# Kernel optimization log

Hardware: AMD Instinct MI355X
Metric: run time of the kernel (lower is better)

## Reference

```python
import jax, jax.numpy as jnp
import numpy as np

EPS = 1e-5
P, B, T, C = 2, 8, 1024, 1024
H = 4 * C

def layernorm(x, g, b):
    mu = jnp.mean(x, axis=-1, keepdims=True)
    var = jnp.var(x, axis=-1, keepdims=True)
    return (x - mu) * jax.lax.rsqrt(var + EPS) * g + b

def time_shift(x):
    # ZeroPad2d((0,0,1,-1)): xx[t] = x[t-1], xx[0] = 0 along the T axis
    pad = [(0, 0)] * (x.ndim - 2) + [(1, 0), (0, 0)]
    return jnp.pad(x, pad)[..., :-1, :]

def wkv(time_decay, time_first, k, v):
    # Faithful port of the RWKV-v4 CUDA WKV scan (numerically stable form).
    # k, v: [N, T, C]; time_decay/time_first: [C]
    w = -jnp.exp(time_decay)  # decay (negative)
    u = time_first
    kT = jnp.moveaxis(k, 1, 0)  # [T, N, C]
    vT = jnp.moveaxis(v, 1, 0)
    N = k.shape[0]
    Cc = k.shape[2]

    def step(carry, kv):
        aa, bb, pp = carry
        kk, vv = kv
        ww = u + kk
        p = jnp.maximum(pp, ww)
        e1 = jnp.exp(pp - p)
        e2 = jnp.exp(ww - p)
        y = (e1 * aa + e2 * vv) / (e1 * bb + e2)
        ww2 = w + pp
        p2 = jnp.maximum(ww2, kk)
        e1b = jnp.exp(ww2 - p2)
        e2b = jnp.exp(kk - p2)
        return (e1b * aa + e2b * vv, e1b * bb + e2b, p2), y

    init = (jnp.zeros((N, Cc), jnp.float32), jnp.zeros((N, Cc), jnp.float32),
            jnp.full((N, Cc), -1e38, jnp.float32))
    _, yT = jax.lax.scan(step, init, (kT, vT))
    return jnp.moveaxis(yT, 0, 1)  # [N, T, C]


def setup_inputs() -> dict:
    key = jax.random.key(0)
    ks = jax.random.split(key, 20)
    f32 = jnp.float32
    layer_id, n_layer = 1, 12
    ratio_0_to_1 = layer_id / (n_layer - 1)
    ratio_1_to_almost0 = 1.0 - layer_id / n_layer
    xcurve = (np.arange(C, dtype=np.float32) / C).reshape(1, 1, C)
    decay_speed = -5 + 8 * (np.arange(C, dtype=np.float32) / (C - 1)) ** (0.7 + 1.3 * ratio_0_to_1)
    zigzag = (np.array([(i + 1) % 3 - 1 for i in range(C)], dtype=np.float32)) * 0.5
    time_first = np.ones(C, dtype=np.float32) * np.log(0.3) + zigzag
    mk = np.stack([xcurve ** ratio_1_to_almost0 for _ in range(P)], 0)  # [P,1,1,C]
    mv = np.stack([xcurve ** ratio_1_to_almost0 + 0.3 * ratio_0_to_1 for _ in range(P)], 0)
    mr = np.stack([xcurve ** (0.5 * ratio_1_to_almost0) for _ in range(P)], 0)
    s = 0.02
    return {
        'x': jax.random.normal(ks[0], (P, B, T, C), f32),
        'ln1_g': jnp.ones((C,), f32), 'ln1_b': jnp.zeros((C,), f32),
        'ln2_g': jnp.ones((C,), f32), 'ln2_b': jnp.zeros((C,), f32),
        'time_decay': jnp.asarray(decay_speed, f32),
        'time_first': jnp.asarray(time_first, f32),
        'att_mix_k': jnp.asarray(mk, f32), 'att_mix_v': jnp.asarray(mv, f32),
        'att_mix_r': jnp.asarray(mr, f32),
        'Wk': jax.random.normal(ks[1], (C, C), f32) * s,
        'Wv': jax.random.normal(ks[2], (C, C), f32) * s,
        'Wr': jax.random.normal(ks[3], (C, C), f32) * s,
        'Wo': jax.random.normal(ks[4], (C, C), f32) * s,
        'cm_mix_k': jnp.asarray(mk, f32), 'cm_mix_r': jnp.asarray(mk, f32),
        'Wck': jax.random.normal(ks[5], (H, C), f32) * s,
        'Wcr': jax.random.normal(ks[6], (C, C), f32) * s,
        'Wcv': jax.random.normal(ks[7], (C, H), f32) * s,
    }


def reference(x, ln1_g, ln1_b, ln2_g, ln2_b, time_decay, time_first,
              att_mix_k, att_mix_v, att_mix_r, Wk, Wv, Wr, Wo,
              cm_mix_k, cm_mix_r, Wck, Wcr, Wcv):
    p, b, t, c = x.shape
    # --- TimeMix branch: x = x + Wo @ (sigmoid(r) * WKV(k, v)) ---
    h = layernorm(x, ln1_g, ln1_b)
    xx = time_shift(h)
    xk = h * att_mix_k + xx * (1 - att_mix_k)
    xv = h * att_mix_v + xx * (1 - att_mix_v)
    xr = h * att_mix_r + xx * (1 - att_mix_r)
    k = jnp.einsum('pbtc,dc->pbtd', xk, Wk)
    v = jnp.einsum('pbtc,dc->pbtd', xv, Wv)
    sr = jax.nn.sigmoid(jnp.einsum('pbtc,dc->pbtd', xr, Wr))
    y = wkv(time_decay, time_first,
            k.reshape(p * b, t, c), v.reshape(p * b, t, c)).reshape(p, b, t, c)
    x = x + jnp.einsum('pbtc,dc->pbtd', sr * y, Wo)
    # --- ChannelMix branch ---
    h = layernorm(x, ln2_g, ln2_b)
    xx = time_shift(h)
    xk = h * cm_mix_k + xx * (1 - cm_mix_k)
    xr = h * cm_mix_r + xx * (1 - cm_mix_r)
    kk = jnp.einsum('pbtc,hc->pbth', xk, Wck)
    kk = jnp.square(jax.nn.relu(kk))
    kv = jnp.einsum('pbth,ch->pbtc', kk, Wcv)
    out = jax.nn.sigmoid(jnp.einsum('pbtc,dc->pbtd', xr, Wcr)) * kv
    return x + out
```

## Files before the change

### kernel.cpp

```cpp
#include <hip/hip_runtime.h>

#define T_SEQ 1024
#define C_DIM 1024
#define H_DIM 4096
#define M_ROWS 16384
#define CHUNKS 16
#define CLEN 64

typedef _Float16 f16x8 __attribute__((ext_vector_type(8)));
typedef _Float16 f16x4 __attribute__((ext_vector_type(4)));
typedef float    f32x4 __attribute__((ext_vector_type(4)));

#define AS1 __attribute__((address_space(1)))
#define AS3 __attribute__((address_space(3)))

__device__ __forceinline__ void gload_lds16(const void* g, void* l) {
  __builtin_amdgcn_global_load_lds((const AS1 void*)g, (AS3 void*)l, 16, 0, 0);
}

__device__ __forceinline__ float sigmoidf_(float x) {
  return 1.0f / (1.0f + __expf(-x));
}

struct CvtArgs {
  const float* src[7];
  _Float16*    dst[7];
  int n4[7];
  int start[8];
};

__global__ __launch_bounds__(256) void cvt_all_kernel(CvtArgs a) {
  const int bid = blockIdx.x;
  int s = 0;
#pragma unroll
  for (int j = 0; j < 7; ++j) s += (bid >= a.start[j + 1]) ? 1 : 0;
  const int i = (bid - a.start[s]) * 256 + threadIdx.x;
  if (i >= a.n4[s]) return;
  f32x4 v = reinterpret_cast<const f32x4*>(a.src[s])[i];
  f16x4 o;
  o[0] = (_Float16)v[0]; o[1] = (_Float16)v[1];
  o[2] = (_Float16)v[2]; o[3] = (_Float16)v[3];
  reinterpret_cast<f16x4*>(a.dst[s])[i] = o;
}

__global__ __launch_bounds__(256) void ln_kernel(const float* __restrict__ x,
    const float* __restrict__ g, const float* __restrict__ b,
    _Float16* __restrict__ h) {
  const int row  = blockIdx.x * 4 + (threadIdx.x >> 6);
  const int lane = threadIdx.x & 63;
  const f32x4* xr = reinterpret_cast<const f32x4*>(x + (size_t)row * C_DIM);
  f32x4 v[4];
  float s = 0.f, sq = 0.f;
#pragma unroll
  for (int i = 0; i < 4; ++i) {
    v[i] = xr[i * 64 + lane];
#pragma unroll
    for (int j = 0; j < 4; ++j) { s += v[i][j]; sq += v[i][j] * v[i][j]; }
  }
#pragma unroll
  for (int off = 32; off > 0; off >>= 1) {
    s  += __shfl_xor(s, off, 64);
    sq += __shfl_xor(sq, off, 64);
  }
  const float mu   = s * (1.0f / C_DIM);
  const float var  = sq * (1.0f / C_DIM) - mu * mu;
  const float rstd = rsqrtf(var + 1e-5f);
  const f32x4* g4 = reinterpret_cast<const f32x4*>(g);
  const f32x4* b4 = reinterpret_cast<const f32x4*>(b);
  f16x4* h4 = reinterpret_cast<f16x4*>(h + (size_t)row * C_DIM);
#pragma unroll
  for (int i = 0; i < 4; ++i) {
    f32x4 gg = g4[i * 64 + lane];
    f32x4 bb = b4[i * 64 + lane];
    f16x4 o;
#pragma unroll
    for (int j = 0; j < 4; ++j)
      o[j] = (_Float16)((v[i][j] - mu) * rstd * gg[j] + bb[j]);
    h4[i * 64 + lane] = o;
  }
}

__global__ __launch_bounds__(256) void mix3_kernel(const _Float16* __restrict__ h,
    const float* __restrict__ mk, const float* __restrict__ mv, const float* __restrict__ mr,
    _Float16* __restrict__ xk, _Float16* __restrict__ xv, _Float16* __restrict__ xr) {
  const int i  = blockIdx.x * 256 + threadIdx.x;
  const int m  = i >> 7;
  const int c0 = (i & 127) << 3;
  const int p  = m >> 13;
  const int t  = m & (T_SEQ - 1);
  const f16x8* h8 = reinterpret_cast<const f16x8*>(h);
  f16x8 hc = h8[i];
  f16x8 hp;
#pragma unroll
  for (int j = 0; j < 8; ++j) hp[j] = (_Float16)0.f;
  if (t) hp = h8[i - 128];
  f16x8 ok, ov, orr;
#pragma unroll
  for (int j = 0; j < 8; ++j) {
    const float hcf = (float)hc[j], hpf = (float)hp[j];
    const float a = mk[p * C_DIM + c0 + j];
    const float c = mv[p * C_DIM + c0 + j];
    const float d = mr[p * C_DIM + c0 + j];
    ok[j]  = (_Float16)(hcf * a + hpf * (1.f - a));
    ov[j]  = (_Float16)(hcf * c + hpf * (1.f - c));
    orr[j] = (_Float16)(hcf * d + hpf * (1.f - d));
  }
  reinterpret_cast<f16x8*>(xk)[i] = ok;
  reinterpret_cast<f16x8*>(xv)[i] = ov;
  reinterpret_cast<f16x8*>(xr)[i] = orr;
}

__global__ __launch_bounds__(256) void mix2_kernel(const _Float16* __restrict__ h,
    const float* __restrict__ mk, const float* __restrict__ mr,
    _Float16* __restrict__ xk, _Float16* __restrict__ xr) {
  const int i  = blockIdx.x * 256 + threadIdx.x;
  const int m  = i >> 7;
  const int c0 = (i & 127) << 3;
  const int p  = m >> 13;
  const int t  = m & (T_SEQ - 1);
  const f16x8* h8 = reinterpret_cast<const f16x8*>(h);
  f16x8 hc = h8[i];
  f16x8 hp;
#pragma unroll
  for (int j = 0; j < 8; ++j) hp[j] = (_Float16)0.f;
  if (t) hp = h8[i - 128];
  f16x8 ok, orr;
#pragma unroll
  for (int j = 0; j < 8; ++j) {
    const float hcf = (float)hc[j], hpf = (float)hp[j];
    const float a = mk[p * C_DIM + c0 + j];
    const float d = mr[p * C_DIM + c0 + j];
    ok[j]  = (_Float16)(hcf * a + hpf * (1.f - a));
    orr[j] = (_Float16)(hcf * d + hpf * (1.f - d));
  }
  reinterpret_cast<f16x8*>(xk)[i] = ok;
  reinterpret_cast<f16x8*>(xr)[i] = orr;
}

__global__ __launch_bounds__(1024, 1) void wkv_kernel(const _Float16* __restrict__ k,
    const _Float16* __restrict__ v, const _Float16* __restrict__ r,
    const float* __restrict__ td, const float* __restrict__ tf,
    _Float16* __restrict__ a_out) {
  __shared__ float sA[CHUNKS][64];
  __shared__ float sB[CHUNKS][64];
  __shared__ float sP[CHUNKS][64];
  const int tid   = threadIdx.x;
  const int chunk = tid >> 6;
  const int ch    = tid & 63;
  const int n     = blockIdx.x >> 4;
  const int cg    = blockIdx.x & 15;
  const int c     = cg * 64 + ch;
  const float w = -__expf(td[c]);
  const float u = tf[c];
  const size_t cbase = (size_t)n * T_SEQ * C_DIM + (size_t)chunk * CLEN * C_DIM + c;

  float aa = 0.f, bb = 0.f, pp = -1e38f;
  for (int s = 0; s < CLEN; ++s) {
    const size_t idx = cbase + (size_t)s * C_DIM;
    const float kk = (float)k[idx];
    const float vv = (float)v[idx];
    const float ww2 = w + pp;
    const float p2  = fmaxf(ww2, kk);
    const float e1b = __expf(ww2 - p2);
    const float e2b = __expf(kk - p2);
    aa = e1b * aa + e2b * vv;
    bb = e1b * bb + e2b;
    pp = p2;
  }
  sA[chunk][ch] = aa; sB[chunk][ch] = bb; sP[chunk][ch] = pp;
  __syncthreads();

  if (chunk == 0) {
    float pa = 0.f, pb = 0.f, ppr = -1e38f;
    const float wL = w * (float)CLEN;
    for (int j = 0; j < CHUNKS; ++j) {
      const float la = sA[j][ch], lb = sB[j][ch], lp = sP[j][ch];
      sA[j][ch] = pa; sB[j][ch] = pb; sP[j][ch] = ppr;
      const float dp = wL + ppr;
      const float np = fmaxf(dp, lp);
      const float e1 = __expf(dp - np);
      const float e2 = __expf(lp - np);
      pa  = e1 * pa + e2 * la;
      pb  = e1 * pb + e2 * lb;
      ppr = np;
    }
  }
  __syncthreads();

  aa = sA[chunk][ch]; bb = sB[chunk][ch]; pp = sP[chunk][ch];
  for (int s = 0; s < CLEN; ++s) {
    const size_t idx = cbase + (size_t)s * C_DIM;
    const float kk = (float)k[idx];
    const float vv = (float)v[idx];
    const float ww = u + kk;
    const float p  = fmaxf(pp, ww);
    const float e1 = __expf(pp - p);
    const float e2 = __expf(ww - p);
    const float yv = __fdividef(e1 * aa + e2 * vv, e1 * bb + e2);
    const float sr = sigmoidf_((float)r[idx]);
    a_out[idx] = (_Float16)(sr * yv);
    const float ww2 = w + pp;
    const float p2  = fmaxf(ww2, kk);
    const float e1b = __expf(ww2 - p2);
    const float e2b = __expf(kk - p2);
    aa = e1b * aa + e2b * vv;
    bb = e1b * bb + e2b;
    pp = p2;
  }
}

#define GBAR() do { __builtin_amdgcn_sched_barrier(0); \
                    __builtin_amdgcn_s_barrier(); \
                    __builtin_amdgcn_sched_barrier(0); } while (0)
#define WVN(n) do { asm volatile("s_waitcnt vmcnt(" #n ")" ::: "memory"); \
                    __builtin_amdgcn_sched_barrier(0); } while (0)
#define WLN(n) do { asm volatile("s_waitcnt lgkmcnt(" #n ")" ::: "memory"); \
                    __builtin_amdgcn_sched_barrier(0); } while (0)
#define SCHED() __builtin_amdgcn_sched_barrier(0)
#define STAGE(op, SRC, row0, k0, bb) do { \
    _Pragma("unroll") \
    for (int c_ = 0; c_ < 2; ++c_) { \
      gload_lds16((SRC) + (size_t)((row0) + c_ * 64) * K + (k0), \
                  &lds[bb][op][((size_t)((row0) + c_ * 64) << 6) + dbase]); \
    } } while (0)
#define RD_AH(dst, mh) do { \
    _Pragma("unroll") for (int i_ = 0; i_ < 4; ++i_) \
    _Pragma("unroll") for (int k_ = 0; k_ < 2; ++k_) \
      dst[i_][k_] = *reinterpret_cast<const f16x8*>( \
        &lds[b][0][((wr * 128 + (mh) * 64 + i_ * 16 + frow) << 6) + \
                   (((k_ << 5) + fk) ^ fxorh)]); \
  } while (0)
#define RD_BALL() do { \
    _Pragma("unroll") for (int j_ = 0; j_ < 4; ++j_) \
    _Pragma("unroll") for (int k_ = 0; k_ < 2; ++k_) \
      bf[j_][k_] = *reinterpret_cast<const f16x8*>( \
        &lds[b][1][((wcn * 64 + j_ * 16 + frow) << 6) + \
                   (((k_ << 5) + fk) ^ fxorh)]); \
  } while (0)
#define MM32(src, mh) do { \
    __builtin_amdgcn_s_setprio(1); \
    _Pragma("unroll") for (int k_ = 0; k_ < 2; ++k_) \
    _Pragma("unroll") for (int i_ = 0; i_ < 4; ++i_) \
    _Pragma("unroll") for (int j_ = 0; j_ < 4; ++j_) \
      acc[(mh) * 4 + i_][j_] = __builtin_amdgcn_mfma_f32_16x16x32_f16( \
        src[i_][k_], bf[j_][k_], acc[(mh) * 4 + i_][j_], 0, 0, 0); \
    __builtin_amdgcn_s_setprio(0); \
  } while (0)

template<int EPI>
__global__ __launch_bounds__(512, 2) void gemm_nt_256(
    const _Float16* __restrict__ A, const _Float16* __restrict__ B,
    void* __restrict__ Cv, const float* __restrict__ X,
    const _Float16* __restrict__ KV, int M, int N, int K) {
  __shared__ _Float16 lds[2][2][256 * 64];
  const int tid  = threadIdx.x;
  const int wave = tid >> 6;
  const int lane = tid & 63;
  const int wr   = wave >> 2;
  const int wcn  = wave & 3;

  const unsigned nwx  = gridDim.x;
  const unsigned pery = gridDim.y >> 3;
  const unsigned id   = blockIdx.y * nwx + blockIdx.x;
  const unsigned xcd  = id & 7;
  const unsigned loc  = id >> 3;
  const size_t m0 = (size_t)(xcd * pery + loc / nwx) * 256;
  const size_t n0 = (size_t)(loc % nwx) * 256;

  const int srow  = tid >> 3;
  const int scolh = ((tid & 7) ^ (srow & 7)) << 3;
  const size_t dbase = (size_t)(srow & ~7) << 6;
  const _Float16* sA = A + (m0 + srow) * (size_t)K + scolh;
  const _Float16* sB = B + (n0 + srow) * (size_t)K + scolh;

  const int frow  = lane & 15;
  const int fk    = (lane >> 4) << 3;
  const int fxorh = (frow & 7) << 3;

  f32x4 acc[8][4];
#pragma unroll
  for (int i = 0; i < 8; ++i)
#pragma unroll
    for (int j = 0; j < 4; ++j) acc[i][j] = (f32x4){0.f, 0.f, 0.f, 0.f};

  STAGE(0, sA, 0, 0, 0); STAGE(0, sA, 128, 0, 0);
  STAGE(1, sB, 0, 0, 0); STAGE(1, sB, 128, 0, 0);

  const int NT = K >> 6;
  for (int t = 0; t < NT; ++t) {
    const int b  = t & 1;
    const int nb = b ^ 1;
    const int k1 = (t + 1) << 6;
    if (t + 1 < NT) {
      STAGE(0, sA, 0, k1, nb); STAGE(0, sA, 128, k1, nb);
      STAGE(1, sB, 0, k1, nb); STAGE(1, sB, 128, k1, nb);
      WVN(8);
    } else {
      WVN(0);
    }
    GBAR();
    f16x8 a0[4][2], a1[4][2], bf[4][2];
    RD_AH(a0, 0); RD_BALL();
    SCHED();
    RD_AH(a1, 1);
    WLN(8);
    MM32(a0, 0);
    WLN(0);
    MM32(a1, 1);
    GBAR();
  }

  const int ecol  = lane & 15;
  const int erow4 = (lane >> 4) * 4;
#pragma unroll
  for (int mf = 0; mf < 8; ++mf)
#pragma unroll
    for (int nf = 0; nf < 4; ++nf) {
      const size_t rbase = m0 + (size_t)(wr * 128 + mf * 16 + erow4);
      const size_t cc    = n0 + (size_t)(wcn * 64 + nf * 16 + ecol);
#pragma unroll
      for (int r = 0; r < 4; ++r) {
        const float val = acc[mf][nf][r];
        const size_t off = (rbase + r) * (size_t)N + cc;
        if constexpr (EPI == 0) {
          ((_Float16*)Cv)[off] = (_Float16)val;
        } else if constexpr (EPI == 1) {
          const float tq = fmaxf(val, 0.f);
          ((_Float16*)Cv)[off] = (_Float16)(tq * tq);
        } else if constexpr (EPI == 2) {
          ((float*)Cv)[off] = val + X[off];
        } else {
          ((float*)Cv)[off] = X[off] + sigmoidf_(val) * (float)KV[off];
        }
      }
    }
}

extern "C" void kernel_launch(void* const* d_in, const int* in_sizes, int n_in,
                              void* d_out, int out_size, void* d_ws, size_t ws_size,
                              hipStream_t stream) {
  const float* x      = (const float*)d_in[0];
  const float* ln1_g  = (const float*)d_in[1];
  const float* ln1_b  = (const float*)d_in[2];
  const float* ln2_g  = (const float*)d_in[3];
  const float* ln2_b  = (const float*)d_in[4];
  const float* tdec   = (const float*)d_in[5];
  const float* tfirst = (const float*)d_in[6];
  const float* amk    = (const float*)d_in[7];
  const float* amv    = (const float*)d_in[8];
  const float* amr    = (const float*)d_in[9];
  const float* Wk     = (const float*)d_in[10];
  const float* Wv     = (const float*)d_in[11];
  const float* Wr     = (const float*)d_in[12];
  const float* Wo     = (const float*)d_in[13];
  const float* cmk    = (const float*)d_in[14];
  const float* cmr    = (const float*)d_in[15];
  const float* Wck    = (const float*)d_in[16];
  const float* Wcr    = (const float*)d_in[17];
  const float* Wcv    = (const float*)d_in[18];

  char* ws = (char*)d_ws;
  const size_t SZ = (size_t)M_ROWS * C_DIM * sizeof(_Float16);
  _Float16* B0 = (_Float16*)(ws + 0 * SZ);
  _Float16* B1 = (_Float16*)(ws + 1 * SZ);
  _Float16* B2 = (_Float16*)(ws + 2 * SZ);
  _Float16* B3 = (_Float16*)(ws + 3 * SZ);
  _Float16* B4 = (_Float16*)(ws + 4 * SZ);
  _Float16* B5 = (_Float16*)(ws + 5 * SZ);
  _Float16* B6 = (_Float16*)(ws + 6 * SZ);
  _Float16* wWk  = (_Float16*)(ws + 7 * SZ);
  _Float16* wWv  = wWk  + (size_t)C_DIM * C_DIM;
  _Float16* wWr  = wWv  + (size_t)C_DIM * C_DIM;
  _Float16* wWo  = wWr  + (size_t)C_DIM * C_DIM;
  _Float16* wWcr = wWo  + (size_t)C_DIM * C_DIM;
  _Float16* wWck = wWcr + (size_t)C_DIM * C_DIM;
  _Float16* wWcv = wWck + (size_t)H_DIM * C_DIM;

  {
    CvtArgs a;
    const float* srcs[7] = {Wk, Wv, Wr, Wo, Wcr, Wck, Wcv};
    _Float16*    dsts[7] = {wWk, wWv, wWr, wWo, wWcr, wWck, wWcv};
    const size_t ns[7]   = {(size_t)C_DIM * C_DIM, (size_t)C_DIM * C_DIM,
                            (size_t)C_DIM * C_DIM, (size_t)C_DIM * C_DIM,
                            (size_t)C_DIM * C_DIM, (size_t)H_DIM * C_DIM,
                            (size_t)C_DIM * H_DIM};
    int st = 0;
    for (int j = 0; j < 7; ++j) {
      a.src[j] = srcs[j]; a.dst[j] = dsts[j];
      a.n4[j] = (int)(ns[j] / 4);
      a.start[j] = st;
      st += (a.n4[j] + 255) / 256;
    }
    a.start[7] = st;
    cvt_all_kernel<<<dim3(st), dim3(256), 0, stream>>>(a);
  }

  const dim3 blk(256);
  const dim3 gblk(512);
  const dim3 gN1(C_DIM / 256, M_ROWS / 256);
  const dim3 gN4(H_DIM / 256, M_ROWS / 256);

  ln_kernel<<<dim3(M_ROWS / 4), blk, 0, stream>>>(x, ln1_g, ln1_b, B0);
  mix3_kernel<<<dim3(M_ROWS * 128 / 256), blk, 0, stream>>>(B0, amk, amv, amr, B1, B2, B3);
  gemm_nt_256<0><<<gN1, gblk, 0, stream>>>(B1, wWk, B4, nullptr, nullptr, M_ROWS, C_DIM, C_DIM);
  gemm_nt_256<0><<<gN1, gblk, 0, stream>>>(B2, wWv, B5, nullptr, nullptr, M_ROWS, C_DIM, C_DIM);
  gemm_nt_256<0><<<gN1, gblk, 0, stream>>>(B3, wWr, B6, nullptr, nullptr, M_ROWS, C_DIM, C_DIM);
  wkv_kernel<<<dim3(256), dim3(1024), 0, stream>>>(B4, B5, B6, tdec, tfirst, B1);
  gemm_nt_256<2><<<gN1, gblk, 0, stream>>>(B1, wWo, d_out, x, nullptr, M_ROWS, C_DIM, C_DIM);

  ln_kernel<<<dim3(M_ROWS / 4), blk, 0, stream>>>((const float*)d_out, ln2_g, ln2_b, B0);
  mix2_kernel<<<dim3(M_ROWS * 128 / 256), blk, 0, stream>>>(B0, cmk, cmr, B1, B2);
  gemm_nt_256<1><<<gN4, gblk, 0, stream>>>(B1, wWck, B3, nullptr, nullptr, M_ROWS, H_DIM, C_DIM);
  gemm_nt_256<0><<<gN1, gblk, 0, stream>>>(B3, wWcv, B1, nullptr, nullptr, M_ROWS, C_DIM, H_DIM);
  gemm_nt_256<3><<<gN1, gblk, 0, stream>>>(B2, wWcr, d_out, (const float*)d_out, B1,
                                           M_ROWS, C_DIM, C_DIM);
}
```

Before: 668.6 us.

## Split GEMM main loop into four quadrant phases interleaving LDS staging with MFMA

Measured after the change: 659.0 us. No clear change (-1.4%).

```diff
diff --git a/kernel.cpp b/kernel.cpp
--- a/kernel.cpp
+++ b/kernel.cpp
@@ -216,7 +216,6 @@
                     __builtin_amdgcn_sched_barrier(0); } while (0)
 #define WLN(n) do { asm volatile("s_waitcnt lgkmcnt(" #n ")" ::: "memory"); \
                     __builtin_amdgcn_sched_barrier(0); } while (0)
-#define SCHED() __builtin_amdgcn_sched_barrier(0)
 #define STAGE(op, SRC, row0, k0, bb) do { \
     _Pragma("unroll") \
     for (int c_ = 0; c_ < 2; ++c_) { \
@@ -227,23 +226,23 @@
     _Pragma("unroll") for (int i_ = 0; i_ < 4; ++i_) \
     _Pragma("unroll") for (int k_ = 0; k_ < 2; ++k_) \
       dst[i_][k_] = *reinterpret_cast<const f16x8*>( \
-        &lds[b][0][((wr * 128 + (mh) * 64 + i_ * 16 + frow) << 6) + \
-                   (((k_ << 5) + fk) ^ fxorh)]); \
+        &lds[bi][0][((wr * 128 + (mh) * 64 + i_ * 16 + frow) << 6) + \
+                    (((k_ << 5) + fk) ^ fxorh)]); \
   } while (0)
-#define RD_BALL() do { \
-    _Pragma("unroll") for (int j_ = 0; j_ < 4; ++j_) \
+#define RD_BH(dst, nh) do { \
+    _Pragma("unroll") for (int j_ = 0; j_ < 2; ++j_) \
     _Pragma("unroll") for (int k_ = 0; k_ < 2; ++k_) \
-      bf[j_][k_] = *reinterpret_cast<const f16x8*>( \
-        &lds[b][1][((wcn * 64 + j_ * 16 + frow) << 6) + \
-                   (((k_ << 5) + fk) ^ fxorh)]); \
+      dst[j_][k_] = *reinterpret_cast<const f16x8*>( \
+        &lds[bi][1][((wcn * 64 + (nh) * 32 + j_ * 16 + frow) << 6) + \
+                    (((k_ << 5) + fk) ^ fxorh)]); \
   } while (0)
-#define MM32(src, mh) do { \
+#define MM16(asrc, bsrc, mh, nh) do { \
     __builtin_amdgcn_s_setprio(1); \
     _Pragma("unroll") for (int k_ = 0; k_ < 2; ++k_) \
     _Pragma("unroll") for (int i_ = 0; i_ < 4; ++i_) \
-    _Pragma("unroll") for (int j_ = 0; j_ < 4; ++j_) \
-      acc[(mh) * 4 + i_][j_] = __builtin_amdgcn_mfma_f32_16x16x32_f16( \
-        src[i_][k_], bf[j_][k_], acc[(mh) * 4 + i_][j_], 0, 0, 0); \
+    _Pragma("unroll") for (int j_ = 0; j_ < 2; ++j_) \
+      acc[(mh) * 4 + i_][(nh) * 2 + j_] = __builtin_amdgcn_mfma_f32_16x16x32_f16( \
+        asrc[i_][k_], bsrc[j_][k_], acc[(mh) * 4 + i_][(nh) * 2 + j_], 0, 0, 0); \
     __builtin_amdgcn_s_setprio(0); \
   } while (0)
 
@@ -288,25 +287,34 @@
 
   const int NT = K >> 6;
   for (int t = 0; t < NT; ++t) {
-    const int b  = t & 1;
-    const int nb = b ^ 1;
+    const int bi = t & 1;
+    const int nb = bi ^ 1;
     const int k1 = (t + 1) << 6;
-    if (t + 1 < NT) {
-      STAGE(0, sA, 0, k1, nb); STAGE(0, sA, 128, k1, nb);
-      STAGE(1, sB, 0, k1, nb); STAGE(1, sB, 128, k1, nb);
-      WVN(8);
-    } else {
-      WVN(0);
-    }
-    GBAR();
-    f16x8 a0[4][2], a1[4][2], bf[4][2];
-    RD_AH(a0, 0); RD_BALL();
-    SCHED();
-    RD_AH(a1, 1);
-    WLN(8);
-    MM32(a0, 0);
+    const bool st = (t + 1) < NT;
+    f16x8 af[4][2], b0f[2][2], b1f[2][2];
+    if (st) { STAGE(0, sA, 0, k1, nb); WVN(2); }
+    else    { WVN(0); }
+    GBAR();
+    RD_AH(af, 0); RD_BH(b0f, 0);
     WLN(0);
-    MM32(a1, 1);
+    MM16(af, b0f, 0, 0);
+    GBAR();
+    RD_BH(b1f, 1);
+    if (st) STAGE(1, sB, 0, k1, nb);
+    GBAR();
+    WLN(0);
+    MM16(af, b1f, 0, 1);
+    GBAR();
+    RD_AH(af, 1);
+    if (st) STAGE(1, sB, 128, k1, nb);
+    GBAR();
+    WLN(0);
+    MM16(af, b0f, 1, 0);
+    GBAR();
+    if (st) STAGE(0, sA, 128, k1, nb);
+    GBAR();
+    WLN(0);
+    MM16(af, b1f, 1, 1);
     GBAR();
   }
 
```

## Batch K/V/R projection GEMMs into one launch and interleave LDS reads with MFMAs

Applied to the files above, without the earlier changes.

Result: no change. 659.5 us (-1.4%).

```diff
diff --git a/kernel.cpp b/kernel.cpp
--- a/kernel.cpp
+++ b/kernel.cpp
@@ -223,27 +223,24 @@
       gload_lds16((SRC) + (size_t)((row0) + c_ * 64) * K + (k0), \
                   &lds[bb][op][((size_t)((row0) + c_ * 64) << 6) + dbase]); \
     } } while (0)
-#define RD_AH(dst, mh) do { \
+#define RD_A4(dst, mh, kk_) do { \
     _Pragma("unroll") for (int i_ = 0; i_ < 4; ++i_) \
-    _Pragma("unroll") for (int k_ = 0; k_ < 2; ++k_) \
-      dst[i_][k_] = *reinterpret_cast<const f16x8*>( \
-        &lds[b][0][((wr * 128 + (mh) * 64 + i_ * 16 + frow) << 6) + \
-                   (((k_ << 5) + fk) ^ fxorh)]); \
+      dst[i_][kk_] = *reinterpret_cast<const f16x8*>( \
+        &lds[bi][0][((wr * 128 + (mh) * 64 + i_ * 16 + frow) << 6) + \
+                    ((((kk_) << 5) + fk) ^ fxorh)]); \
   } while (0)
-#define RD_BALL() do { \
+#define RD_B4(kk_) do { \
     _Pragma("unroll") for (int j_ = 0; j_ < 4; ++j_) \
-    _Pragma("unroll") for (int k_ = 0; k_ < 2; ++k_) \
-      bf[j_][k_] = *reinterpret_cast<const f16x8*>( \
-        &lds[b][1][((wcn * 64 + j_ * 16 + frow) << 6) + \
-                   (((k_ << 5) + fk) ^ fxorh)]); \
+      bf[j_][kk_] = *reinterpret_cast<const f16x8*>( \
+        &lds[bi][1][((wcn * 64 + j_ * 16 + frow) << 6) + \
+                    ((((kk_) << 5) + fk) ^ fxorh)]); \
   } while (0)
-#define MM32(src, mh) do { \
+#define MMC(asrc, kk_, half) do { \
     __builtin_amdgcn_s_setprio(1); \
-    _Pragma("unroll") for (int k_ = 0; k_ < 2; ++k_) \
     _Pragma("unroll") for (int i_ = 0; i_ < 4; ++i_) \
     _Pragma("unroll") for (int j_ = 0; j_ < 4; ++j_) \
-      acc[(mh) * 4 + i_][j_] = __builtin_amdgcn_mfma_f32_16x16x32_f16( \
-        src[i_][k_], bf[j_][k_], acc[(mh) * 4 + i_][j_], 0, 0, 0); \
+      acc[(half) * 4 + i_][j_] = __builtin_amdgcn_mfma_f32_16x16x32_f16( \
+        asrc[i_][kk_], bf[j_][kk_], acc[(half) * 4 + i_][j_], 0, 0, 0); \
     __builtin_amdgcn_s_setprio(0); \
   } while (0)
 
@@ -251,13 +248,18 @@
 __global__ __launch_bounds__(512, 2) void gemm_nt_256(
     const _Float16* __restrict__ A, const _Float16* __restrict__ B,
     void* __restrict__ Cv, const float* __restrict__ X,
-    const _Float16* __restrict__ KV, int M, int N, int K) {
+    const _Float16* __restrict__ KV, int M, int N, int K,
+    size_t strideA, size_t strideB, size_t strideCbytes) {
   __shared__ _Float16 lds[2][2][256 * 64];
   const int tid  = threadIdx.x;
   const int wave = tid >> 6;
   const int lane = tid & 63;
   const int wr   = wave >> 2;
   const int wcn  = wave & 3;
+
+  A  = A + (size_t)blockIdx.z * strideA;
+  B  = B + (size_t)blockIdx.z * strideB;
+  Cv = (void*)((char*)Cv + (size_t)blockIdx.z * strideCbytes);
 
   const unsigned nwx  = gridDim.x;
   const unsigned pery = gridDim.y >> 3;
@@ -288,8 +290,8 @@
 
   const int NT = K >> 6;
   for (int t = 0; t < NT; ++t) {
-    const int b  = t & 1;
-    const int nb = b ^ 1;
+    const int bi = t & 1;
+    const int nb = bi ^ 1;
     const int k1 = (t + 1) << 6;
     if (t + 1 < NT) {
       STAGE(0, sA, 0, k1, nb); STAGE(0, sA, 128, k1, nb);
@@ -300,13 +302,20 @@
     }
     GBAR();
     f16x8 a0[4][2], a1[4][2], bf[4][2];
-    RD_AH(a0, 0); RD_BALL();
-    SCHED();
-    RD_AH(a1, 1);
+    RD_A4(a0, 0, 0); SCHED();
+    RD_B4(0);        SCHED();
+    RD_A4(a0, 0, 1); SCHED();
+    RD_B4(1);        SCHED();
     WLN(8);
-    MM32(a0, 0);
+    MMC(a0, 0, 0);
+    RD_A4(a1, 1, 0); SCHED();
+    WLN(4);
+    MMC(a0, 1, 0);
+    RD_A4(a1, 1, 1); SCHED();
+    WLN(4);
+    MMC(a1, 0, 1);
     WLN(0);
-    MM32(a1, 1);
+    MMC(a1, 1, 1);
     GBAR();
   }
 
@@ -398,20 +407,25 @@
   const dim3 blk(256);
   const dim3 gblk(512);
   const dim3 gN1(C_DIM / 256, M_ROWS / 256);
+  const dim3 gKVR(C_DIM / 256, M_ROWS / 256, 3);
   const dim3 gN4(H_DIM / 256, M_ROWS / 256);
 
   ln_kernel<<<dim3(M_ROWS / 4), blk, 0, stream>>>(x, ln1_g, ln1_b, B0);
   mix3_kernel<<<dim3(M_ROWS * 128 / 256), blk, 0, stream>>>(B0, amk, amv, amr, B1, B2, B3);
-  gemm_nt_256<0><<<gN1, gblk, 0, stream>>>(B1, wWk, B4, nullptr, nullptr, M_ROWS, C_DIM, C_DIM);
-  gemm_nt_256<0><<<gN1, gblk, 0, stream>>>(B2, wWv, B5, nullptr, nullptr, M_ROWS, C_DIM, C_DIM);
-  gemm_nt_256<0><<<gN1, gblk, 0, stream>>>(B3, wWr, B6, nullptr, nullptr, M_ROWS, C_DIM, C_DIM);
+  gemm_nt_256<0><<<gKVR, gblk, 0, stream>>>(B1, wWk, B4, nullptr, nullptr,
+      M_ROWS, C_DIM, C_DIM,
+      (size_t)M_ROWS * C_DIM, (size_t)C_DIM * C_DIM,
+      (size_t)M_ROWS * C_DIM * sizeof(_Float16));
   wkv_kernel<<<dim3(256), dim3(1024), 0, stream>>>(B4, B5, B6, tdec, tfirst, B1);
-  gemm_nt_256<2><<<gN1, gblk, 0, stream>>>(B1, wWo, d_out, x, nullptr, M_ROWS, C_DIM, C_DIM);
+  gemm_nt_256<2><<<gN1, gblk, 0, stream>>>(B1, wWo, d_out, x, nullptr,
+      M_ROWS, C_DIM, C_DIM, 0, 0, 0);
 
   ln_kernel<<<dim3(M_ROWS / 4), blk, 0, stream>>>((const float*)d_out, ln2_g, ln2_b, B0);
   mix2_kernel<<<dim3(M_ROWS * 128 / 256), blk, 0, stream>>>(B0, cmk, cmr, B1, B2);
-  gemm_nt_256<1><<<gN4, gblk, 0, stream>>>(B1, wWck, B3, nullptr, nullptr, M_ROWS, H_DIM, C_DIM);
-  gemm_nt_256<0><<<gN1, gblk, 0, stream>>>(B3, wWcv, B1, nullptr, nullptr, M_ROWS, C_DIM, H_DIM);
+  gemm_nt_256<1><<<gN4, gblk, 0, stream>>>(B1, wWck, B3, nullptr, nullptr,
+      M_ROWS, H_DIM, C_DIM, 0, 0, 0);
+  gemm_nt_256<0><<<gN1, gblk, 0, stream>>>(B3, wWcv, B1, nullptr, nullptr,
+      M_ROWS, C_DIM, H_DIM, 0, 0, 0);
   gemm_nt_256<3><<<gN1, gblk, 0, stream>>>(B2, wWcr, d_out, (const float*)d_out, B1,
-                                           M_ROWS, C_DIM, C_DIM);
-}
+      M_ROWS, C_DIM, C_DIM, 0, 0, 0);
+}
```
